# Kernel tuning notes

Hardware: AMD Instinct MI355X
Metric: run time of the kernel (lower is better)

## Reference

```python
import jax, jax.numpy as jnp
import numpy as np

B, T_ENC, T_DEC = 32, 512, 512
N_MELS, PRENET, ENC_H, ATTN_H, DEC_H, ATTN_D, N_FILT, KSIZE = 80, 256, 512, 1024, 1024, 128, 32, 31


def _lstm_cell(x, h, c, wih, whh, bih, bhh):
    gates = x @ wih.T + h @ whh.T + bih + bhh  # (B, 4H)
    i, f, g, o = jnp.split(gates, 4, axis=-1)  # torch LSTMCell gate order
    c2 = jax.nn.sigmoid(f) * c + jax.nn.sigmoid(i) * jnp.tanh(g)
    h2 = jax.nn.sigmoid(o) * jnp.tanh(c2)
    return h2, c2


def setup_inputs() -> dict:
    key = jax.random.key(0)
    ks = jax.random.split(key, 24)
    s = lambda k, shape, scale: jax.random.normal(k, shape, dtype=jnp.float32) * scale
    inp = {
        'encoder_output': s(ks[0], (B, T_ENC, ENC_H), 1.0),
        'targets': s(ks[1], (B, T_DEC, N_MELS), 1.0),
        'prenet_w1': s(ks[2], (PRENET, N_MELS), 0.05),
        'prenet_b1': jnp.zeros((PRENET,), jnp.float32),
        'prenet_w2': s(ks[3], (PRENET, PRENET), 0.05),
        'prenet_b2': jnp.zeros((PRENET,), jnp.float32),
        'M_w': s(ks[4], (ATTN_D, ENC_H), 0.04),
        'Q_w': s(ks[5], (ATTN_D, ATTN_H), 0.03),
        'W_w': s(ks[6], (1, ATTN_D), 0.08),
        'L_w': s(ks[7], (ATTN_D, N_FILT), 0.1),
        'conv_w': s(ks[8], (N_FILT, 2, KSIZE), 0.1),
        'attn_wih': s(ks[9], (4 * ATTN_H, ENC_H + PRENET), 0.02),
        'attn_whh': s(ks[10], (4 * ATTN_H, ATTN_H), 0.02),
        'attn_bih': jnp.zeros((4 * ATTN_H,), jnp.float32),
        'attn_bhh': jnp.zeros((4 * ATTN_H,), jnp.float32),
        'dec_wih': s(ks[11], (4 * DEC_H, ATTN_H + ENC_H), 0.02),
        'dec_whh': s(ks[12], (4 * DEC_H, DEC_H), 0.02),
        'dec_bih': jnp.zeros((4 * DEC_H,), jnp.float32),
        'dec_bhh': jnp.zeros((4 * DEC_H,), jnp.float32),
        'proj_w': s(ks[13], (N_MELS, DEC_H + ENC_H), 0.02),
        'proj_b': jnp.zeros((N_MELS,), jnp.float32),
    }
    return inp


def _decoder(encoder_output, targets, prenet_w1, prenet_b1, prenet_w2, prenet_b2,
             M_w, Q_w, W_w, L_w, conv_w,
             attn_wih, attn_whh, attn_bih, attn_bhh,
             dec_wih, dec_whh, dec_bih, dec_bhh, proj_w, proj_b):
    b, t_enc, _ = encoder_output.shape
    t_dec = targets.shape[1]
    pad = (KSIZE - 1) // 2

    # prenet over [zeros ; targets][:, :t_dec]  (eval mode: dropout off)
    dec_in = jnp.concatenate([jnp.zeros((b, 1, N_MELS), targets.dtype), targets], axis=1)[:, :t_dec]
    h = jax.nn.relu(dec_in @ prenet_w1.T + prenet_b1)
    prenet_out = jax.nn.relu(h @ prenet_w2.T + prenet_b2)  # (B, T_dec, prenet)

    processed_enc = encoder_output @ M_w.T  # (B, T_enc, attn_dim)

    def step(carry, x):
        ah, ac, dh, dc, aw, aws, ctx = carry
        # attention LSTM
        cell_in = jnp.concatenate([x, ctx], axis=-1)
        ah, ac = _lstm_cell(cell_in, ah, ac, attn_wih, attn_whh, attn_bih, attn_bhh)
        # location-sensitive attention
        prev_attn = jnp.stack([aw, aws], axis=1)  # (B, 2, T_enc)
        pa = jax.lax.conv_general_dilated(prev_attn, conv_w, (1,), [(pad, pad)],
                                          dimension_numbers=('NCH', 'OIH', 'NCH'))  # (B, F, T)
        pa = jnp.einsum('bft,df->btd', pa, L_w)  # (B, T, attn_dim)
        q = (ah @ Q_w.T)[:, None, :]  # (B, 1, attn_dim)
        energies = jnp.tanh(q + processed_enc + pa) @ W_w[0]  # (B, T)
        aw = jax.nn.softmax(energies, axis=1)
        ctx = jnp.einsum('bt,bte->be', aw, encoder_output)
        aws = aws + aw
        # decoder LSTM
        dcell_in = jnp.concatenate([ah, ctx], axis=-1)
        dh, dc = _lstm_cell(dcell_in, dh, dc, dec_wih, dec_whh, dec_bih, dec_bhh)
        out = jnp.concatenate([dh, ctx], axis=-1) @ proj_w.T + proj_b  # (B, n_mels)
        return (ah, ac, dh, dc, aw, aws, ctx), (out, aw)

    z = lambda d: jnp.zeros((b, d), encoder_output.dtype)
    carry0 = (z(ATTN_H), z(ATTN_H), z(DEC_H), z(DEC_H), z(t_enc), z(t_enc), z(ENC_H))
    xs = jnp.swapaxes(prenet_out, 0, 1)  # (T_dec, B, prenet)
    _, (mels, aligns) = jax.lax.scan(step, carry0, xs)
    mel_outputs = jnp.swapaxes(mels, 0, 1)      # (B, T_dec, n_mels)
    alignments = jnp.swapaxes(aligns, 0, 1)     # (B, T_dec, T_enc)
    return mel_outputs, alignments


def reference(encoder_output, targets, prenet_w1, prenet_b1, prenet_w2, prenet_b2,
              M_w, Q_w, W_w, L_w, conv_w,
              attn_wih, attn_whh, attn_bih, attn_bhh,
              dec_wih, dec_whh, dec_bih, dec_bhh, proj_w, proj_b):
    return _decoder(encoder_output, targets, prenet_w1, prenet_b1, prenet_w2, prenet_b2,
                    M_w, Q_w, W_w, L_w, conv_w,
                    attn_wih, attn_whh, attn_bih, attn_bhh,
                    dec_wih, dec_whh, dec_bih, dec_bhh, proj_w, proj_b)
```

## Files before the change

### kernel.cpp

```cpp
#include <hip/hip_runtime.h>
#include <hip/hip_fp16.h>
#include <cstddef>

typedef unsigned int uint32;

#define B_   32
#define TE_  512
#define TD_  512
#define NM_  80
#define PRE_ 256
#define EH_  512
#define AH_  1024
#define AD_  128

__device__ __forceinline__ float sigf(float x) { return 1.0f / (1.0f + expf(-x)); }

__device__ __forceinline__ float agl(const float* p) {
  return __hip_atomic_load(p, __ATOMIC_RELAXED, __HIP_MEMORY_SCOPE_AGENT);
}
__device__ __forceinline__ void ags(float* p, float v) {
  __hip_atomic_store(p, v, __ATOMIC_RELAXED, __HIP_MEMORY_SCOPE_AGENT);
}
__device__ __forceinline__ float4 agl4(const float* p) {
  float4 r; r.x = agl(p); r.y = agl(p + 1); r.z = agl(p + 2); r.w = agl(p + 3);
  return r;
}

__device__ __forceinline__ void gsync(uint32* bar, unsigned bep) {
  __syncthreads();
  if (threadIdx.x == 0) {
    asm volatile("s_waitcnt vmcnt(0)" ::: "memory");
    uint32* leaf = bar + (blockIdx.x >> 5) * 32;
    uint32* root = bar + 256;
    uint32 prev = __hip_atomic_fetch_add(leaf, 1u, __ATOMIC_RELAXED, __HIP_MEMORY_SCOPE_AGENT);
    if (prev + 1u == 32u * bep)
      __hip_atomic_fetch_add(root, 1u, __ATOMIC_RELAXED, __HIP_MEMORY_SCOPE_AGENT);
    int spins = 0;
    while (__hip_atomic_load(root, __ATOMIC_RELAXED, __HIP_MEMORY_SCOPE_AGENT) < 8u * bep) {
      __builtin_amdgcn_s_sleep(2);
      if (++spins > 20000000) break;
    }
  }
  __syncthreads();
}

__device__ __forceinline__ float rowsum16(float v) {
  int vi;
  vi = __float_as_int(v);
  v += __int_as_float(__builtin_amdgcn_update_dpp(0, vi, 0xB1, 0xF, 0xF, true));
  vi = __float_as_int(v);
  v += __int_as_float(__builtin_amdgcn_update_dpp(0, vi, 0x4E, 0xF, 0xF, true));
  vi = __float_as_int(v);
  v += __int_as_float(__builtin_amdgcn_update_dpp(0, vi, 0x124, 0xF, 0xF, true));
  vi = __float_as_int(v);
  v += __int_as_float(__builtin_amdgcn_update_dpp(0, vi, 0x128, 0xF, 0xF, true));
  return v;
}

__global__ __launch_bounds__(256) void k_pack_lstm2(
    const float* __restrict__ awih, const float* __restrict__ awhh,
    const float* __restrict__ dwih, const float* __restrict__ dwhh,
    uint32* __restrict__ wal, uint32* __restrict__ wdl, uint32* __restrict__ wdt)
{
  long gid = blockIdx.x * 256L + threadIdx.x;
  const long N1 = 3686400L, N2 = 4603904L, N3 = 655360L;
  if (gid < N1) {
    int blk = (int)(gid / 28800), rem = (int)(gid % 28800);
    int r2 = rem % 900;
    int ks = rem / 900;
    uint32 out = 0;
    if (r2 < 896) {
      int kq = r2 >> 4, rd = r2 & 15;
      int k = kq * 32 + ks;
      int rp0 = blk * 32 + 2 * rd, rp1 = rp0 + 1;
      int row0 = (rp0 & 3) * 1024 + (rp0 >> 2);
      int row1 = (rp1 & 3) * 1024 + (rp1 >> 2);
      float w0 = (k < 768) ? awih[(size_t)row0 * 768 + k] : awhh[(size_t)row0 * 1024 + k - 768];
      float w1 = (k < 768) ? awih[(size_t)row1 * 768 + k] : awhh[(size_t)row1 * 1024 + k - 768];
      __half2 h = __floats2half2_rn(w0, w1);
      out = *(uint32*)&h;
    }
    wal[gid] = out;
  } else if (gid < N1 + N2) {
    long g = gid - N1;
    int blk = (int)(g / 35968), rem = (int)(g % 35968);
    int r2 = rem % 1124;
    int ks = rem / 1124;
    uint32 out = 0;
    if (r2 < 1120) {
      int kq = r2 >> 4, rd = r2 & 15;
      int k = kq * 32 + ks;
      int rp0 = blk * 32 + 2 * rd, rp1 = rp0 + 1;
      int row0 = (rp0 & 3) * 1024 + (rp0 >> 2);
      int row1 = (rp1 & 3) * 1024 + (rp1 >> 2);
      float w0 = (k < 1536) ? dwih[(size_t)row0 * 1536 + k] : dwhh[(size_t)row0 * 1024 + k - 1536];
      float w1 = (k < 1536) ? dwih[(size_t)row1 * 1536 + k] : dwhh[(size_t)row1 * 1024 + k - 1536];
      __half2 h = __floats2half2_rn(w0, w1);
      out = *(uint32*)&h;
    }
    wdl[g] = out;
  } else if (gid < N1 + N2 + N3) {
    long g = gid - N1 - N2;
    int blk = (int)(g / 5120), rem = (int)(g % 5120);
    int rd2 = rem & 3, rg = (rem >> 2) & 3, ks = (rem >> 4) & 31, i = rem >> 9;
    int k = 2240 + 32 * i + ks;
    int r0 = rg * 8 + 2 * rd2;
    int rp0 = blk * 32 + r0, rp1 = rp0 + 1;
    int row0 = (rp0 & 3) * 1024 + (rp0 >> 2);
    int row1 = (rp1 & 3) * 1024 + (rp1 >> 2);
    float w0 = (k < 1536) ? dwih[(size_t)row0 * 1536 + k] : dwhh[(size_t)row0 * 1024 + k - 1536];
    float w1 = (k < 1536) ? dwih[(size_t)row1 * 1536 + k] : dwhh[(size_t)row1 * 1024 + k - 1536];
    __half2 h = __floats2half2_rn(w0, w1);
    wdt[g] = *(uint32*)&h;
  }
}

__global__ __launch_bounds__(256) void k_pack_small(
    const float* __restrict__ w1, const float* __restrict__ w2,
    const float* __restrict__ mw, const float* __restrict__ pw,
    const float* __restrict__ abih, const float* __restrict__ abhh,
    const float* __restrict__ dbih, const float* __restrict__ dbhh,
    const float* __restrict__ lw, const float* __restrict__ cw,
    float* __restrict__ w1t, float* __restrict__ w2t, float* __restrict__ mt,
    float* __restrict__ pjt, float* __restrict__ ba, float* __restrict__ bd,
    float* __restrict__ lc)
{
  int gid = blockIdx.x * 256 + threadIdx.x;
  if (gid < 20480) { int k = gid / 256, j = gid % 256; w1t[gid] = w1[j * 80 + k]; return; }
  gid -= 20480;
  if (gid < 65536) { int k = gid / 256, j = gid % 256; w2t[gid] = w2[j * 256 + k]; return; }
  gid -= 65536;
  if (gid < 65536) { int e = gid / 128, d = gid % 128; mt[gid] = mw[d * 512 + e]; return; }
  gid -= 65536;
  if (gid < 122880) { int k = gid / 80, m = gid % 80; pjt[gid] = pw[m * 1536 + k]; return; }
  gid -= 122880;
  if (gid < 4096) { int j = gid >> 2, g = gid & 3, row = g * 1024 + j; ba[gid] = abih[row] + abhh[row]; return; }
  gid -= 4096;
  if (gid < 4096) { int j = gid >> 2, g = gid & 3, row = g * 1024 + j; bd[gid] = dbih[row] + dbhh[row]; return; }
  gid -= 4096;
  if (gid < 7936) {
    int c = gid / (31 * 128), rem = gid % (31 * 128);
    int kk = rem / 128, d = rem % 128;
    float s = 0.f;
    for (int f = 0; f < 32; ++f) s += lw[d * 32 + f] * cw[(f * 2 + c) * 31 + kk];
    lc[gid] = s;
  }
}

__global__ __launch_bounds__(256) void k_prenet(
    const float* __restrict__ targets, const float* __restrict__ w1t,
    const float* __restrict__ b1, const float* __restrict__ w2t,
    const float* __restrict__ b2, float* __restrict__ pn)
{
  int t = blockIdx.x, tid = threadIdx.x;
  __shared__ float X[32][80];
  __shared__ float h1[256][33];
  for (int i = tid; i < 2560; i += 256) {
    int b = i / 80, m = i % 80;
    X[b][m] = (t == 0) ? 0.f : targets[((size_t)b * TD_ + (t - 1)) * NM_ + m];
  }
  __syncthreads();
  int j = tid;
  float bj = b1[j];
  for (int bt = 0; bt < 4; ++bt) {
    float acc[8];
#pragma unroll
    for (int i = 0; i < 8; ++i) acc[i] = bj;
    for (int k = 0; k < 80; ++k) {
      float w = w1t[k * 256 + j];
#pragma unroll
      for (int i = 0; i < 8; ++i) acc[i] += w * X[bt * 8 + i][k];
    }
#pragma unroll
    for (int i = 0; i < 8; ++i) h1[j][bt * 8 + i] = fmaxf(acc[i], 0.f);
  }
  __syncthreads();
  float cj = b2[j];
  float* out = pn + (size_t)t * PRE_ * B_;
  for (int bt = 0; bt < 4; ++bt) {
    float acc[8];
#pragma unroll
    for (int i = 0; i < 8; ++i) acc[i] = cj;
    for (int k = 0; k < 256; ++k) {
      float w = w2t[k * 256 + j];
#pragma unroll
      for (int i = 0; i < 8; ++i) acc[i] += w * h1[k][bt * 8 + i];
    }
#pragma unroll
    for (int i = 0; i < 8; ++i) out[j * 32 + bt * 8 + i] = fmaxf(acc[i], 0.f);
  }
}

__global__ __launch_bounds__(256) void k_penc(
    const float* __restrict__ enc, const float* __restrict__ mt,
    float* __restrict__ penc)
{
  int t = blockIdx.x, tid = threadIdx.x;
  __shared__ float encL[32][256];
  __shared__ float red[128][8][2];
  int d = tid & 127, s = tid >> 7;
  float acc[4][8];
#pragma unroll
  for (int bt = 0; bt < 4; ++bt)
#pragma unroll
    for (int i = 0; i < 8; ++i) acc[bt][i] = 0.f;
  for (int eh = 0; eh < 2; ++eh) {
    for (int i = tid; i < 8192; i += 256) {
      int b = i >> 8, e = i & 255;
      encL[b][e] = enc[((size_t)b * TE_ + t) * EH_ + eh * 256 + e];
    }
    __syncthreads();
    for (int bt = 0; bt < 4; ++bt) {
      for (int el = s * 128; el < s * 128 + 128; ++el) {
        float w = mt[(eh * 256 + el) * 128 + d];
#pragma unroll
        for (int i = 0; i < 8; ++i) acc[bt][i] += w * encL[bt * 8 + i][el];
      }
    }
    __syncthreads();
  }
  for (int bt = 0; bt < 4; ++bt) {
#pragma unroll
    for (int i = 0; i < 8; ++i) red[d][i][s] = acc[bt][i];
    __syncthreads();
    if (s == 0) {
#pragma unroll
      for (int i = 0; i < 8; ++i)
        penc[((size_t)t * AD_ + d) * 32 + bt * 8 + i] = red[d][i][0] + red[d][i][1];
    }
    __syncthreads();
  }
}

__global__ __launch_bounds__(256) void k_enct(
    const float* __restrict__ enc, __half* __restrict__ enct)
{
  int blk = blockIdx.x, tid = threadIdx.x;
  int b = blk >> 6, t0 = ((blk >> 3) & 7) * 64, e0 = (blk & 7) * 64;
  __shared__ float tile[64][65];
  for (int i = 0; i < 16; ++i) {
    int tl = i * 4 + (tid >> 6), e = tid & 63;
    tile[tl][e] = enc[((size_t)b * TE_ + t0 + tl) * EH_ + e0 + e];
  }
  __syncthreads();
  for (int i = 0; i < 16; ++i) {
    int el = i * 4 + (tid >> 6), tl = tid & 63;
    enct[((size_t)b * EH_ + e0 + el) * TE_ + t0 + tl] = __float2half(tile[tl][el]);
  }
}

struct KP {
  const uint32* wal; const uint32* wdl; const uint4* wdt;
  const float* pn; const float* penc; const __half* enct;
  const float* qw; const float* ww; const float* pjt; const float* pjb;
  const float* lc; const float* ba; const float* bd;
  float* ahv; float* ac; float* dhv; float* dc; float* ctxv;
  float* awv; float* awsv;
  float* enp; float* mel; float* align;
  uint32* bar; int pv;
};

__device__ __forceinline__ void fma2(uint4 wv, const float* __restrict__ XC,
                                     int xb, float* acc)
{
  const __half2* hp = (const __half2*)&wv;
  float w[8];
#pragma unroll
  for (int d = 0; d < 4; ++d) {
    float2 f = __half22float2(hp[d]);
    w[2 * d] = f.x; w[2 * d + 1] = f.y;
  }
  float4 xa = *(const float4*)&XC[xb];
  float4 xc2 = *(const float4*)&XC[xb + 4];
  float x[8] = {xa.x, xa.y, xa.z, xa.w, xc2.x, xc2.y, xc2.z, xc2.w};
#pragma unroll
  for (int ri = 0; ri < 8; ++ri)
#pragma unroll
    for (int bi = 0; bi < 8; ++bi)
      acc[ri * 8 + bi] = fmaf(w[ri], x[bi], acc[ri * 8 + bi]);
}

__device__ __forceinline__ void lstm_finish(
    float* acc, float* __restrict__ GT, const float* __restrict__ bias,
    float* __restrict__ cst, float* __restrict__ hout,
    int rp0, int tid, int ks, int bq, int rg)
{
#pragma unroll
  for (int i = 0; i < 64; ++i) {
    float v = rowsum16(acc[i]);
    acc[i] = v + __shfl_xor(v, 16);
  }
  if (ks == 0) {
#pragma unroll
    for (int ri = 0; ri < 8; ++ri) {
      *(float4*)&GT[(rg * 8 + ri) * 32 + bq * 8] =
          make_float4(acc[ri * 8 + 0], acc[ri * 8 + 1], acc[ri * 8 + 2], acc[ri * 8 + 3]);
      *(float4*)&GT[(rg * 8 + ri) * 32 + bq * 8 + 4] =
          make_float4(acc[ri * 8 + 4], acc[ri * 8 + 5], acc[ri * 8 + 6], acc[ri * 8 + 7]);
    }
  }
  __syncthreads();
  if (tid < 256) {
    int jl = tid >> 5, b = tid & 31;
    float gi = GT[(jl * 4 + 0) * 32 + b] + bias[rp0 + jl * 4 + 0];
    float gf = GT[(jl * 4 + 1) * 32 + b] + bias[rp0 + jl * 4 + 1];
    float gg = GT[(jl * 4 + 2) * 32 + b] + bias[rp0 + jl * 4 + 2];
    float go = GT[(jl * 4 + 3) * 32 + b] + bias[rp0 + jl * 4 + 3];
    int j = (rp0 >> 2) + jl;
    float c0 = cst[j * 32 + b];
    float c2 = sigf(gf) * c0 + sigf(gi) * tanhf(gg);
    float h2 = sigf(go) * tanhf(c2);
    cst[j * 32 + b] = c2;
    ags(&hout[j * 32 + b], h2);
  }
}

__device__ __forceinline__ void run_lstm_a(const KP& p, int t,
    const float* __restrict__ ah_in, const float* __restrict__ ctx_in,
    float* __restrict__ ah_out,
    uint32* WlU, float* XC, float* GT, int tid, int ks, int bq, int rg,
    int kidx, int b4, int blk)
{
  float acc[64];
#pragma unroll
  for (int i = 0; i < 64; ++i) acc[i] = 0.f;
  const float* xp0 = p.pn + (size_t)t * 8192;
  const int wb = ks * 900 + rg * 4;
  const int xr = ks * 36 + bq * 8;
  auto ldA = [&](int kg) -> float4 {
    if (kg < 256) return *(const float4*)(xp0 + (size_t)kg * 32 + b4);
    if (kg < 768) return agl4(ctx_in + (size_t)(kg - 256) * 32 + b4);
    return agl4(ah_in + (size_t)(kg - 768) * 32 + b4);
  };
  float4 st0 = ldA(kidx);
  float4 st1 = ldA(64 + kidx);
  for (int cb = 0; cb < 28; cb += 2) {
    __syncthreads();
    *(float4*)&XC[kidx * 36 + b4] = st0;
    __syncthreads();
    if (cb + 2 < 28) st0 = ldA((cb + 2) * 64 + kidx);
    fma2(*(const uint4*)&WlU[wb + (2 * cb) * 16], XC, xr, acc);
    fma2(*(const uint4*)&WlU[wb + (2 * cb + 1) * 16], XC, xr + 32 * 36, acc);
    __syncthreads();
    *(float4*)&XC[kidx * 36 + b4] = st1;
    __syncthreads();
    if (cb + 3 < 28) st1 = ldA((cb + 3) * 64 + kidx);
    fma2(*(const uint4*)&WlU[wb + (2 * cb + 2) * 16], XC, xr, acc);
    fma2(*(const uint4*)&WlU[wb + (2 * cb + 3) * 16], XC, xr + 32 * 36, acc);
  }
  lstm_finish(acc, GT, p.ba, p.ac, ah_out, blk * 32, tid, ks, bq, rg);
}

__device__ __forceinline__ void run_lstm_d(const KP& p,
    const float* __restrict__ xp0, const float* __restrict__ xp1,
    const float* __restrict__ xp2, float* __restrict__ dh_w,
    uint32* WlU, float* XC, float* GT,
    int tid, int ks, int bq, int rg, int kidx, int b4, int blk)
{
  float acc[64];
#pragma unroll
  for (int i = 0; i < 64; ++i) acc[i] = 0.f;
  const int wb = ks * 1124 + rg * 4;
  const int xr = ks * 36 + bq * 8;
  auto ldD = [&](int kg) -> float4 {
    const float* s = (kg < 1024) ? xp0 + (size_t)kg * 32
                   : (kg < 1536) ? xp1 + (size_t)(kg - 1024) * 32
                                 : xp2 + (size_t)(kg - 1536) * 32;
    return agl4(s + b4);
  };
  float4 st0 = ldD(kidx);
  float4 st1 = ldD(64 + kidx);
  for (int cb = 0; cb < 32; cb += 2) {
    __syncthreads();
    *(float4*)&XC[kidx * 36 + b4] = st0;
    __syncthreads();
    st0 = ldD((cb + 2) * 64 + kidx);
    fma2(*(const uint4*)&WlU[wb + (2 * cb) * 16], XC, xr, acc);
    fma2(*(const uint4*)&WlU[wb + (2 * cb + 1) * 16], XC, xr + 32 * 36, acc);
    __syncthreads();
    *(float4*)&XC[kidx * 36 + b4] = st1;
    __syncthreads();
    st1 = ldD((cb + 3) * 64 + kidx);
    fma2(*(const uint4*)&WlU[wb + (2 * cb + 2) * 16], XC, xr, acc);
    fma2(*(const uint4*)&WlU[wb + (2 * cb + 3) * 16], XC, xr + 32 * 36, acc);
  }
  const uint4* wg = p.wdt + (size_t)(blk - 128) * 1280;
  const int wi = ks * 4 + rg;
  uint4 twA0, twB0, twA1, twB1;
  __syncthreads(); *(float4*)&XC[kidx * 36 + b4] = st0; __syncthreads();
  st0 = ldD(34 * 64 + kidx);
  twA0 = wg[0 * 128 + wi]; twB0 = wg[1 * 128 + wi];
  fma2(*(const uint4*)&WlU[wb + 64 * 16], XC, xr, acc);
  fma2(*(const uint4*)&WlU[wb + 65 * 16], XC, xr + 32 * 36, acc);
  __syncthreads(); *(float4*)&XC[kidx * 36 + b4] = st1; __syncthreads();
  st1 = ldD(35 * 64 + kidx);
  twA1 = wg[2 * 128 + wi]; twB1 = wg[3 * 128 + wi];
  fma2(*(const uint4*)&WlU[wb + 66 * 16], XC, xr, acc);
  fma2(*(const uint4*)&WlU[wb + 67 * 16], XC, xr + 32 * 36, acc);
  __syncthreads(); *(float4*)&XC[kidx * 36 + b4] = st0; __syncthreads();
  st0 = ldD(36 * 64 + kidx);
  fma2(*(const uint4*)&WlU[wb + 68 * 16], XC, xr, acc);
  fma2(*(const uint4*)&WlU[wb + 69 * 16], XC, xr + 32 * 36, acc);
  __syncthreads(); *(float4*)&XC[kidx * 36 + b4] = st1; __syncthreads();
  st1 = ldD(37 * 64 + kidx);
  fma2(twA0, XC, xr, acc); fma2(twB0, XC, xr + 32 * 36, acc);
  twA0 = wg[4 * 128 + wi]; twB0 = wg[5 * 128 + wi];
  __syncthreads(); *(float4*)&XC[kidx * 36 + b4] = st0; __syncthreads();
  st0 = ldD(38 * 64 + kidx);
  fma2(twA1, XC, xr, acc); fma2(twB1, XC, xr + 32 * 36, acc);
  twA1 = wg[6 * 128 + wi]; twB1 = wg[7 * 128 + wi];
  __syncthreads(); *(float4*)&XC[kidx * 36 + b4] = st1; __syncthreads();
  st1 = ldD(39 * 64 + kidx);
  fma2(twA0, XC, xr, acc); fma2(twB0, XC, xr + 32 * 36, acc);
  twA0 = wg[8 * 128 + wi]; twB0 = wg[9 * 128 + wi];
  __syncthreads(); *(float4*)&XC[kidx * 36 + b4] = st0; __syncthreads();
  fma2(twA1, XC, xr, acc); fma2(twB1, XC, xr + 32 * 36, acc);
  __syncthreads(); *(float4*)&XC[kidx * 36 + b4] = st1; __syncthreads();
  fma2(twA0, XC, xr, acc); fma2(twB0, XC, xr + 32 * 36, acc);
  lstm_finish(acc, GT, p.bd, p.dc, dh_w, (blk - 128) * 32, tid, ks, bq, rg);
}

__device__ __forceinline__ void mel_block(
    const float* __restrict__ dhp, const float* __restrict__ ctp,
    const float* __restrict__ pjt, const float* __restrict__ pjb,
    float* __restrict__ mel, int bb, int tt, float* S, int tid)
{
  float* xo = S + 1536;
  float* ro = S + 3072;
  for (int i = tid; i < 1536; i += 512)
    xo[i] = (i < 1024) ? agl(&dhp[i * 32 + bb]) : agl(&ctp[(i - 1024) * 32 + bb]);
  __syncthreads();
  if (tid < 480) {
    int m = tid % 80, k2 = tid / 80;
    float a2 = 0.f;
    for (int k = k2 * 256; k < k2 * 256 + 256; ++k) a2 += pjt[k * 80 + m] * xo[k];
    ro[m * 8 + k2] = a2;
  }
  __syncthreads();
  if (tid < 80) {
    float s3 = pjb[tid];
#pragma unroll
    for (int k = 0; k < 6; ++k) s3 += ro[tid * 8 + k];
    mel[((size_t)bb * TD_ + tt) * NM_ + tid] = s3;
  }
}

__global__ __launch_bounds__(512) void k_step(KP p)
{
  __shared__ float LDSF[40432];
  const int blk = blockIdx.x, tid = threadIdx.x;
  const int ks = tid & 31, bq = (tid >> 5) & 3, rg = tid >> 7;
  const int kidx = tid >> 3, b4 = (tid & 7) * 4;
  const bool isA = blk < 128;
  float* SC = LDSF + (isA ? 28800 : 35968);
  float* XC = SC;
  float* GT = SC + 2304;
  uint32* WlU = (uint32*)LDSF;
  unsigned bep = 0;

  {
    const uint32* src = isA ? p.wal + (size_t)blk * 28800
                            : p.wdl + (size_t)(blk - 128) * 35968;
    int n4 = isA ? 7200 : 8992;
    for (int i = tid; i < n4; i += 512)
      ((uint4*)WlU)[i] = ((const uint4*)src)[i];
  }
  __syncthreads();

  for (int t = 0; t < TD_; ++t) {
    const int vc = t % p.pv;
    const int vn = (t + 1) % p.pv;
    const int vp = (t > 0) ? (t - 1) % p.pv : 0;
    const float* ah_in  = p.ahv + (size_t)vc * 32768;
    float*       ah_out = p.ahv + (size_t)vn * 32768;
    const float* ctx_in = p.ctxv + (size_t)vc * 16384;
    float*       ctx_out= p.ctxv + (size_t)vn * 16384;

    if (isA) {
      run_lstm_a(p, t, ah_in, ctx_in, ah_out, WlU, XC, GT, tid, ks, bq, rg, kidx, b4, blk);
    } else if (t > 0) {
      run_lstm_d(p, ah_in, ctx_in,
                 p.dhv + (size_t)vp * 32768, p.dhv + (size_t)vc * 32768,
                 WlU, XC, GT, tid, ks, bq, rg, kidx, b4, blk);
    }
    bep += 1; gsync(p.bar, bep);
    {
      int tc = blk >> 3, ds = blk & 7;
      int t0 = tc * 16, d0 = ds * 16;
      float* qs  = SC;
      float* wws = SC + 512;
      float* AHC = SC + 528;
      float* win = SC + 528;
      float* lcs = SC + 528 + 2944;

      const float* awsrc  = p.awv  + (size_t)vc * 16384;
      const float* awssrc = p.awsv + (size_t)vc * 16384;
      float winr[6];
#pragma unroll
      for (int k = 0; k < 6; ++k) {
        int i = tid + k * 512;
        float v = 0.f;
        if (i < 2944) {
          int c = i / 1472, r = (i >> 5) % 46, bbw = i & 31;
          int tg = t0 - 15 + r;
          if (tg >= 0 && tg < 512) v = agl((c ? awssrc : awsrc) + tg * 32 + bbw);
        }
        winr[k] = v;
      }
      float lcr[2];
#pragma unroll
      for (int k = 0; k < 2; ++k) {
        int i = tid + k * 512;
        lcr[k] = 0.f;
        if (i < 992) {
          int c = i / 496, kk = (i >> 4) % 31, dl2 = i & 15;
          lcr[k] = p.lc[(c * 31 + kk) * 128 + d0 + dl2];
        }
      }
      const int bbE = tid & 31, thE = tid >> 5;
      const int ttE = t0 + thE;
      float pencr[16];
#pragma unroll
      for (int dl2 = 0; dl2 < 16; ++dl2)
        pencr[dl2] = p.penc[((size_t)ttE * 128 + d0 + dl2) * 32 + bbE];
      float wwr = (tid < 16) ? p.ww[d0 + tid] : 0.f;

      int bb2 = tid & 31, dl = tid >> 5;
      const float* ahsrc = p.ahv + (size_t)vn * 32768;
      const float* qbase = p.qw + (size_t)(d0 + dl) * 1024;
      float qacc = 0.f;
      float4 sq0 = agl4(ahsrc + 0 * 2048 + tid * 4);
      float4 sq1 = agl4(ahsrc + 1 * 2048 + tid * 4);
      for (int cb = 0; cb < 16; cb += 2) {
        __syncthreads();
        *(float4*)(AHC + tid * 4) = sq0;
        __syncthreads();
        if (cb + 2 < 16) sq0 = agl4(ahsrc + (cb + 2) * 2048 + tid * 4);
        {
          const float* qrow = qbase + cb * 64;
#pragma unroll
          for (int jj = 0; jj < 64; jj += 4) {
            float4 qv = *(const float4*)(qrow + jj);
            qacc = fmaf(qv.x, AHC[(jj + 0) * 32 + bb2], qacc);
            qacc = fmaf(qv.y, AHC[(jj + 1) * 32 + bb2], qacc);
            qacc = fmaf(qv.z, AHC[(jj + 2) * 32 + bb2], qacc);
            qacc = fmaf(qv.w, AHC[(jj + 3) * 32 + bb2], qacc);
          }
        }
        __syncthreads();
        *(float4*)(AHC + tid * 4) = sq1;
        __syncthreads();
        if (cb + 3 < 16) sq1 = agl4(ahsrc + (cb + 3) * 2048 + tid * 4);
        {
          const float* qrow = qbase + (cb + 1) * 64;
#pragma unroll
          for (int jj = 0; jj < 64; jj += 4) {
            float4 qv = *(const float4*)(qrow + jj);
            qacc = fmaf(qv.x, AHC[(jj + 0) * 32 + bb2], qacc);
            qacc = fmaf(qv.y, AHC[(jj + 1) * 32 + bb2], qacc);
            qacc = fmaf(qv.z, AHC[(jj + 2) * 32 + bb2], qacc);
            qacc = fmaf(qv.w, AHC[(jj + 3) * 32 + bb2], qacc);
          }
        }
      }
      __syncthreads();
      qs[dl * 32 + bb2] = qacc;
      if (tid < 16) wws[tid] = wwr;
#pragma unroll
      for (int k = 0; k < 6; ++k) { int i = tid + k * 512; if (i < 2944) win[i] = winr[k]; }
#pragma unroll
      for (int k = 0; k < 2; ++k) { int i = tid + k * 512; if (i < 992) lcs[i] = lcr[k]; }
      __syncthreads();
      {
        float pa[16];
#pragma unroll
        for (int i = 0; i < 16; ++i) pa[i] = 0.f;
        for (int c = 0; c < 2; ++c) {
          for (int kk = 0; kk < 31; ++kk) {
            float wv = win[c * 1472 + (thE + kk) * 32 + bbE];
            const float4* lr = (const float4*)(lcs + c * 496 + kk * 16);
            float4 l0 = lr[0], l1 = lr[1], l2 = lr[2], l3 = lr[3];
            pa[0]  += l0.x * wv; pa[1]  += l0.y * wv; pa[2]  += l0.z * wv; pa[3]  += l0.w * wv;
            pa[4]  += l1.x * wv; pa[5]  += l1.y * wv; pa[6]  += l1.z * wv; pa[7]  += l1.w * wv;
            pa[8]  += l2.x * wv; pa[9]  += l2.y * wv; pa[10] += l2.z * wv; pa[11] += l2.w * wv;
            pa[12] += l3.x * wv; pa[13] += l3.y * wv; pa[14] += l3.z * wv; pa[15] += l3.w * wv;
          }
        }
        float epv = 0.f;
#pragma unroll
        for (int dl2 = 0; dl2 < 16; ++dl2) {
          float v = qs[dl2 * 32 + bbE] + pencr[dl2] + pa[dl2];
          epv += wws[dl2] * tanhf(v);
        }
        ags(&p.enp[(size_t)bbE * 4096 + ttE * 8 + ds], epv);
      }
    }
    bep += 1; gsync(p.bar, bep);
    {
      int bb = blk >> 3, et = blk & 7;
      float* awL = SC + 512;
      float* cr  = SC + 1024;
      int el = tid & 63, ts = tid >> 6;
      const uint32* eb = (const uint32*)(p.enct +
          ((size_t)(bb * 512 + et * 64 + el)) * 512 + ts * 64);
      uint32 ebr[32];
#pragma unroll
      for (int i = 0; i < 32; ++i) ebr[i] = eb[i];
      const float* epb = p.enp + (size_t)bb * 4096 + tid * 8;
      float e = agl(epb) + agl(epb + 1) + agl(epb + 2) + agl(epb + 3)
              + agl(epb + 4) + agl(epb + 5) + agl(epb + 6) + agl(epb + 7);
      float m = e;
#pragma unroll
      for (int k = 1; k < 64; k <<= 1) m = fmaxf(m, __shfl_xor(m, k));
      int wv = tid >> 6;
      if ((tid & 63) == 0) SC[wv] = m;
      __syncthreads();
      m = SC[0];
#pragma unroll
      for (int k = 1; k < 8; ++k) m = fmaxf(m, SC[k]);
      float x = expf(e - m);
      float s = x;
#pragma unroll
      for (int k = 1; k < 64; k <<= 1) s += __shfl_xor(s, k);
      if ((tid & 63) == 0) SC[8 + wv] = s;
      __syncthreads();
      s = SC[8];
#pragma unroll
      for (int k = 1; k < 8; ++k) s += SC[8 + k];
      float a = x * (1.f / s);
      awL[tid] = a;
      __syncthreads();
      float acc = 0.f;
#pragma unroll
      for (int i = 0; i < 32; ++i) {
        float2 f = __half22float2(*(const __half2*)&ebr[i]);
        acc += awL[ts * 64 + 2 * i] * f.x + awL[ts * 64 + 2 * i + 1] * f.y;
      }
      cr[ts * 64 + el] = acc;
      __syncthreads();
      if (tid < 64) {
        float s2 = 0.f;
#pragma unroll
        for (int k = 0; k < 8; ++k) s2 += cr[k * 64 + tid];
        ags(&ctx_out[(et * 64 + tid) * 32 + bb], s2);
      }
      if (et == 0) {
        float osv = agl(&p.awsv[(size_t)vc * 16384 + tid * 32 + bb]);
        ags(&p.awv[(size_t)vn * 16384 + tid * 32 + bb], a);
        ags(&p.awsv[(size_t)vn * 16384 + tid * 32 + bb], osv + a);
        p.align[((size_t)bb * TD_ + t) * TE_ + tid] = a;
      }
      if (et == 1 && t > 0) {
        mel_block(p.dhv + (size_t)vc * 32768, p.ctxv + (size_t)vc * 16384,
                  p.pjt, p.pjb, p.mel, bb, t - 1, SC, tid);
      }
    }
    bep += 1; gsync(p.bar, bep);
  }
  {
    const int v511 = 511 % p.pv, v512 = 512 % p.pv;
    if (!isA) {
      run_lstm_d(p, p.ahv + (size_t)v512 * 32768, p.ctxv + (size_t)v512 * 16384,
                 p.dhv + (size_t)v511 * 32768, p.dhv + (size_t)v512 * 32768,
                 WlU, XC, GT, tid, ks, bq, rg, kidx, b4, blk);
    }
    bep += 1; gsync(p.bar, bep);
    if (blk < 32) {
      mel_block(p.dhv + (size_t)v512 * 32768, p.ctxv + (size_t)v512 * 16384,
                p.pjt, p.pjb, p.mel, blk, 511, SC, tid);
    }
  }
}

extern "C" void kernel_launch(void* const* d_in, const int* in_sizes, int n_in,
                              void* d_out, int out_size, void* d_ws, size_t ws_size,
                              hipStream_t stream)
{
  const float* enc     = (const float*)d_in[0];
  const float* targets = (const float*)d_in[1];
  const float* pw1  = (const float*)d_in[2];
  const float* pb1  = (const float*)d_in[3];
  const float* pw2  = (const float*)d_in[4];
  const float* pb2  = (const float*)d_in[5];
  const float* mw   = (const float*)d_in[6];
  const float* qw   = (const float*)d_in[7];
  const float* www  = (const float*)d_in[8];
  const float* lw   = (const float*)d_in[9];
  const float* cw   = (const float*)d_in[10];
  const float* awih = (const float*)d_in[11];
  const float* awhh = (const float*)d_in[12];
  const float* abih = (const float*)d_in[13];
  const float* abhh = (const float*)d_in[14];
  const float* dwih = (const float*)d_in[15];
  const float* dwhh = (const float*)d_in[16];
  const float* dbih = (const float*)d_in[17];
  const float* dbhh = (const float*)d_in[18];
  const float* pjw  = (const float*)d_in[19];
  const float* pjb  = (const float*)d_in[20];

  uint32* wsb = (uint32*)d_ws;
  size_t o = 0;
  auto F = [&](size_t n) { size_t r = o; o += n; return r; };
  size_t oWAL = F(3686400), oWDL = F(4603904), oWDT = F(655360);
  size_t oENCT = F(4194304);
  size_t oPN = F(4194304), oPENC = F(2097152);
  size_t oW1T = F(20480), oW2T = F(65536), oMT = F(65536), oPJT = F(122880);
  size_t oLC = F(7936), oBA = F(4096), oBD = F(4096);
  size_t oZR = o;
  size_t oAC = F(32768), oDC = F(32768), oBAR = F(1024);
  size_t zr_dw = o - oZR;
  o = (o + 31) & ~(size_t)31;
  size_t fixed_dw = o;
  size_t avail_dw = ws_size / 4;
  long pvl = (avail_dw > fixed_dw) ? (long)((avail_dw - fixed_dw) / 114688) : 0;
  int pv = (pvl < 3) ? 3 : (pvl > 513 ? 513 : (int)pvl);
  size_t oAHV  = F((size_t)pv * 32768);
  size_t oDHV  = F((size_t)pv * 32768);
  size_t oCTXV = F((size_t)pv * 16384);
  size_t oAWV  = F((size_t)pv * 16384);
  size_t oAWSV = F((size_t)pv * 16384);
  size_t oENP  = oW1T;

  hipMemsetAsync(wsb + oZR, 0, zr_dw * 4, stream);
  hipMemsetAsync(wsb + oAHV, 0, (size_t)32768 * 4, stream);
  hipMemsetAsync(wsb + oDHV, 0, (size_t)32768 * 4, stream);
  hipMemsetAsync(wsb + oCTXV, 0, (size_t)16384 * 4, stream);
  hipMemsetAsync(wsb + oAWV, 0, (size_t)16384 * 4, stream);
  hipMemsetAsync(wsb + oAWSV, 0, (size_t)16384 * 4, stream);

  float* mel = (float*)d_out;
  float* align = mel + (size_t)B_ * TD_ * NM_;

  k_pack_lstm2<<<34944, 256, 0, stream>>>(awih, awhh, dwih, dwhh,
                                          wsb + oWAL, wsb + oWDL, wsb + oWDT);
  k_pack_small<<<1135, 256, 0, stream>>>(pw1, pw2, mw, pjw, abih, abhh, dbih, dbhh,
                                         lw, cw,
                                         (float*)(wsb + oW1T), (float*)(wsb + oW2T),
                                         (float*)(wsb + oMT), (float*)(wsb + oPJT),
                                         (float*)(wsb + oBA), (float*)(wsb + oBD),
                                         (float*)(wsb + oLC));
  k_prenet<<<512, 256, 0, stream>>>(targets, (float*)(wsb + oW1T), pb1,
                                    (float*)(wsb + oW2T), pb2, (float*)(wsb + oPN));
  k_penc<<<512, 256, 0, stream>>>(enc, (float*)(wsb + oMT), (float*)(wsb + oPENC));
  k_enct<<<2048, 256, 0, stream>>>(enc, (__half*)(wsb + oENCT));

  KP kp;
  kp.wal = wsb + oWAL; kp.wdl = wsb + oWDL; kp.wdt = (const uint4*)(wsb + oWDT);
  kp.pn = (float*)(wsb + oPN); kp.penc = (float*)(wsb + oPENC);
  kp.enct = (__half*)(wsb + oENCT);
  kp.qw = qw; kp.ww = www; kp.pjt = (float*)(wsb + oPJT); kp.pjb = pjb;
  kp.lc = (float*)(wsb + oLC); kp.ba = (float*)(wsb + oBA); kp.bd = (float*)(wsb + oBD);
  kp.ahv = (float*)(wsb + oAHV); kp.ac = (float*)(wsb + oAC);
  kp.dhv = (float*)(wsb + oDHV); kp.dc = (float*)(wsb + oDC);
  kp.ctxv = (float*)(wsb + oCTXV);
  kp.awv = (float*)(wsb + oAWV); kp.awsv = (float*)(wsb + oAWSV);
  kp.enp = (float*)(wsb + oENP); kp.mel = mel; kp.align = align;
  kp.bar = wsb + oBAR; kp.pv = pv;

  void* kargs[] = { &kp };
  hipLaunchCooperativeKernel((const void*)k_step, dim3(256), dim3(512), kargs,
                             0, stream);
}
```

Measured before the change: 113.2 ms.

## Fuse attention query projection into attention-LSTM epilogue via atomic accumulation

Each attention-LSTM block now multiplies its freshly computed 8 hidden units by a cached slice of Q_w and atomically adds the partial query into a 4-slot ring buffer. The attention-energy phase then reads the finished query value directly, so it no longer re-reads the whole hidden state and Q_w and redoes a 1024-long dot product. Ring slots are cleared two steps ahead inside the softmax phase. Atomic loads are also widened to 64-bit pairs. In exchange it adds float atomic contention and a nondeterministic summation order.

```diff
diff --git a/kernel.cpp b/kernel.cpp
--- a/kernel.cpp
+++ b/kernel.cpp
@@ -3,6 +3,7 @@
 #include <cstddef>
 
 typedef unsigned int uint32;
+typedef unsigned long long u64;
 
 #define B_   32
 #define TE_  512
@@ -22,8 +23,15 @@
   __hip_atomic_store(p, v, __ATOMIC_RELAXED, __HIP_MEMORY_SCOPE_AGENT);
 }
 __device__ __forceinline__ float4 agl4(const float* p) {
-  float4 r; r.x = agl(p); r.y = agl(p + 1); r.z = agl(p + 2); r.w = agl(p + 3);
+  u64 a = __hip_atomic_load((const u64*)p, __ATOMIC_RELAXED, __HIP_MEMORY_SCOPE_AGENT);
+  u64 b = __hip_atomic_load(((const u64*)p) + 1, __ATOMIC_RELAXED, __HIP_MEMORY_SCOPE_AGENT);
+  float4 r;
+  r.x = __uint_as_float((uint32)a); r.y = __uint_as_float((uint32)(a >> 32));
+  r.z = __uint_as_float((uint32)b); r.w = __uint_as_float((uint32)(b >> 32));
   return r;
+}
+__device__ __forceinline__ void agadd(float* p, float v) {
+  __hip_atomic_fetch_add(p, v, __ATOMIC_RELAXED, __HIP_MEMORY_SCOPE_AGENT);
 }
 
 __device__ __forceinline__ void gsync(uint32* bar, unsigned bep) {
@@ -256,7 +264,7 @@
   const float* lc; const float* ba; const float* bd;
   float* ahv; float* ac; float* dhv; float* dc; float* ctxv;
   float* awv; float* awsv;
-  float* enp; float* mel; float* align;
+  float* enp; float* qv; float* mel; float* align;
   uint32* bar; int pv;
 };
 
@@ -282,7 +290,7 @@
 
 __device__ __forceinline__ void lstm_finish(
     float* acc, float* __restrict__ GT, const float* __restrict__ bias,
-    float* __restrict__ cst, float* __restrict__ hout,
+    float* __restrict__ cst, float* __restrict__ hout, float* __restrict__ hl,
     int rp0, int tid, int ks, int bq, int rg)
 {
 #pragma unroll
@@ -312,6 +320,7 @@
     float h2 = sigf(go) * tanhf(c2);
     cst[j * 32 + b] = c2;
     ags(&hout[j * 32 + b], h2);
+    if (hl) hl[jl * 32 + b] = h2;
   }
 }
 
@@ -348,7 +357,25 @@
     fma2(*(const uint4*)&WlU[wb + (2 * cb + 2) * 16], XC, xr, acc);
     fma2(*(const uint4*)&WlU[wb + (2 * cb + 3) * 16], XC, xr + 32 * 36, acc);
   }
-  lstm_finish(acc, GT, p.ba, p.ac, ah_out, blk * 32, tid, ks, bq, rg);
+  float* HL = XC + 3328;
+  lstm_finish(acc, GT, p.ba, p.ac, ah_out, HL, blk * 32, tid, ks, bq, rg);
+  __syncthreads();
+  {
+    const float* QWL = XC + 4608;
+    const int d = tid >> 2, bg = (tid & 3) * 8;
+    float qa[8];
+#pragma unroll
+    for (int i = 0; i < 8; ++i) qa[i] = 0.f;
+#pragma unroll
+    for (int jl = 0; jl < 8; ++jl) {
+      float w = QWL[d * 8 + jl];
+#pragma unroll
+      for (int i = 0; i < 8; ++i) qa[i] = fmaf(w, HL[jl * 32 + bg + i], qa[i]);
+    }
+    float* qdst = p.qv + (size_t)(t & 3) * 4096 + d * 32 + bg;
+#pragma unroll
+    for (int i = 0; i < 8; ++i) agadd(qdst + i, qa[i]);
+  }
 }
 
 __device__ __forceinline__ void run_lstm_d(const KP& p,
@@ -417,7 +444,7 @@
   fma2(twA1, XC, xr, acc); fma2(twB1, XC, xr + 32 * 36, acc);
   __syncthreads(); *(float4*)&XC[kidx * 36 + b4] = st1; __syncthreads();
   fma2(twA0, XC, xr, acc); fma2(twB0, XC, xr + 32 * 36, acc);
-  lstm_finish(acc, GT, p.bd, p.dc, dh_w, (blk - 128) * 32, tid, ks, bq, rg);
+  lstm_finish(acc, GT, p.bd, p.dc, dh_w, nullptr, (blk - 128) * 32, tid, ks, bq, rg);
 }
 
 __device__ __forceinline__ void mel_block(
@@ -465,6 +492,11 @@
     for (int i = tid; i < n4; i += 512)
       ((uint4*)WlU)[i] = ((const uint4*)src)[i];
   }
+  if (isA) {
+    float* QWL = SC + 4608;
+    for (int i = tid; i < 1024; i += 512)
+      QWL[i] = p.qw[(size_t)(i >> 3) * 1024 + blk * 8 + (i & 7)];
+  }
   __syncthreads();
 
   for (int t = 0; t < TD_; ++t) {
@@ -489,10 +521,11 @@
       int t0 = tc * 16, d0 = ds * 16;
       float* qs  = SC;
       float* wws = SC + 512;
-      float* AHC = SC + 528;
       float* win = SC + 528;
       float* lcs = SC + 528 + 2944;
 
+      int bb2 = tid & 31, dl = tid >> 5;
+      float qvv = agl(p.qv + (size_t)(t & 3) * 4096 + (d0 + dl) * 32 + bb2);
       const float* awsrc  = p.awv  + (size_t)vc * 16384;
       const float* awssrc = p.awsv + (size_t)vc * 16384;
       float winr[6];
@@ -525,46 +558,7 @@
         pencr[dl2] = p.penc[((size_t)ttE * 128 + d0 + dl2) * 32 + bbE];
       float wwr = (tid < 16) ? p.ww[d0 + tid] : 0.f;
 
-      int bb2 = tid & 31, dl = tid >> 5;
-      const float* ahsrc = p.ahv + (size_t)vn * 32768;
-      const float* qbase = p.qw + (size_t)(d0 + dl) * 1024;
-      float qacc = 0.f;
-      float4 sq0 = agl4(ahsrc + 0 * 2048 + tid * 4);
-      float4 sq1 = agl4(ahsrc + 1 * 2048 + tid * 4);
-      for (int cb = 0; cb < 16; cb += 2) {
-        __syncthreads();
-        *(float4*)(AHC + tid * 4) = sq0;
-        __syncthreads();
-        if (cb + 2 < 16) sq0 = agl4(ahsrc + (cb + 2) * 2048 + tid * 4);
-        {
-          const float* qrow = qbase + cb * 64;
-#pragma unroll
-          for (int jj = 0; jj < 64; jj += 4) {
-            float4 qv = *(const float4*)(qrow + jj);
-            qacc = fmaf(qv.x, AHC[(jj + 0) * 32 + bb2], qacc);
-            qacc = fmaf(qv.y, AHC[(jj + 1) * 32 + bb2], qacc);
-            qacc = fmaf(qv.z, AHC[(jj + 2) * 32 + bb2], qacc);
-            qacc = fmaf(qv.w, AHC[(jj + 3) * 32 + bb2], qacc);
-          }
-        }
-        __syncthreads();
-        *(float4*)(AHC + tid * 4) = sq1;
-        __syncthreads();
-        if (cb + 3 < 16) sq1 = agl4(ahsrc + (cb + 3) * 2048 + tid * 4);
-        {
-          const float* qrow = qbase + (cb + 1) * 64;
-#pragma unroll
-          for (int jj = 0; jj < 64; jj += 4) {
-            float4 qv = *(const float4*)(qrow + jj);
-            qacc = fmaf(qv.x, AHC[(jj + 0) * 32 + bb2], qacc);
-            qacc = fmaf(qv.y, AHC[(jj + 1) * 32 + bb2], qacc);
-            qacc = fmaf(qv.z, AHC[(jj + 2) * 32 + bb2], qacc);
-            qacc = fmaf(qv.w, AHC[(jj + 3) * 32 + bb2], qacc);
-          }
-        }
-      }
-      __syncthreads();
-      qs[dl * 32 + bb2] = qacc;
+      qs[dl * 32 + bb2] = qvv;
       if (tid < 16) wws[tid] = wwr;
 #pragma unroll
       for (int k = 0; k < 6; ++k) { int i = tid + k * 512; if (i < 2944) win[i] = winr[k]; }
@@ -607,8 +601,10 @@
 #pragma unroll
       for (int i = 0; i < 32; ++i) ebr[i] = eb[i];
       const float* epb = p.enp + (size_t)bb * 4096 + tid * 8;
-      float e = agl(epb) + agl(epb + 1) + agl(epb + 2) + agl(epb + 3)
-              + agl(epb + 4) + agl(epb + 5) + agl(epb + 6) + agl(epb + 7);
+      float4 e0 = agl4(epb), e1 = agl4(epb + 4);
+      float e = e0.x + e0.y + e0.z + e0.w + e1.x + e1.y + e1.z + e1.w;
+      if (et == 3 && tid < 128)
+        ags(p.qv + (size_t)((t + 2) & 3) * 4096 + bb * 128 + tid, 0.f);
       float m = e;
 #pragma unroll
       for (int k = 1; k < 64; k <<= 1) m = fmaxf(m, __shfl_xor(m, k));
@@ -707,7 +703,7 @@
   size_t oW1T = F(20480), oW2T = F(65536), oMT = F(65536), oPJT = F(122880);
   size_t oLC = F(7936), oBA = F(4096), oBD = F(4096);
   size_t oZR = o;
-  size_t oAC = F(32768), oDC = F(32768), oBAR = F(1024);
+  size_t oAC = F(32768), oDC = F(32768), oQV = F(16384), oBAR = F(1024);
   size_t zr_dw = o - oZR;
   o = (o + 31) & ~(size_t)31;
   size_t fixed_dw = o;
@@ -754,7 +750,8 @@
   kp.dhv = (float*)(wsb + oDHV); kp.dc = (float*)(wsb + oDC);
   kp.ctxv = (float*)(wsb + oCTXV);
   kp.awv = (float*)(wsb + oAWV); kp.awsv = (float*)(wsb + oAWSV);
-  kp.enp = (float*)(wsb + oENP); kp.mel = mel; kp.align = align;
+  kp.enp = (float*)(wsb + oENP); kp.qv = (float*)(wsb + oQV);
+  kp.mel = mel; kp.align = align;
   kp.bar = wsb + oBAR; kp.pv = pv;
 
   void* kargs[] = { &kp };
```

Measured after the change: 97.94 ms. 1.16x faster.
